# Kernel tuning notes

Hardware: AMD Instinct MI355X
Metric: run time of the kernel (lower is better)

Reference implementation:

```python
import jax, jax.numpy as jnp
import numpy as np

B, S, D, DQKV = 4, 2048, 1024, 1024

def setup_inputs() -> dict:
    key = jax.random.key(0)
    kx, kq, kk, kv = jax.random.split(key, 4)
    scale = 1.0 / np.sqrt(D)
    return {
        "x": jax.random.normal(kx, (B, S, D), dtype=jnp.float32),
        "wq": jax.random.normal(kq, (D, DQKV), dtype=jnp.float32) * scale,
        "wk": jax.random.normal(kk, (D, DQKV), dtype=jnp.float32) * scale,
        "wv": jax.random.normal(kv, (D, DQKV), dtype=jnp.float32) * scale,
    }

def reference(x, wq, wk, wv):
    # QKV projections: [B,S,D] @ [D,Dqkv] -> [B,S,Dqkv]
    q = jnp.einsum('bsd,de->bse', x, wq)
    k = jnp.einsum('bsd,de->bse', x, wk)
    v = jnp.einsum('bsd,de->bse', x, wv)
    # scores: [B,S,S], scaled by sqrt(dim_qkv)
    scores = jnp.einsum('bik,bjk->bij', q, k) / jnp.sqrt(jnp.asarray(DQKV, dtype=x.dtype))
    attn = jax.nn.softmax(scores, axis=-1)
    # output: [B,S,Dqkv]
    return jnp.einsum('bij,bjd->bid', attn, v)
```

## Files before the change

kernel.cpp:

```cpp
#include <hip/hip_runtime.h>
#include <cstdint>
#include <cstddef>

typedef __bf16 bf16;
typedef __bf16 bf16x4 __attribute__((ext_vector_type(4)));
typedef __bf16 bf16x8 __attribute__((ext_vector_type(8)));
typedef float  f32x4  __attribute__((ext_vector_type(4)));
typedef float  f32x16 __attribute__((ext_vector_type(16)));

#define BATCH 4
#define SEQ   2048
#define DIM   1024
#define LDP   2112

__device__ __forceinline__ bf16 to_bf16(float f) {
    unsigned u = __builtin_bit_cast(unsigned, f);
    u += 0x7fffu + ((u >> 16) & 1u);
    unsigned short h = (unsigned short)(u >> 16);
    return __builtin_bit_cast(bf16, h);
}

__device__ __forceinline__ void load16_lds(const bf16* g, bf16* l) {
    __builtin_amdgcn_global_load_lds(
        (__attribute__((address_space(1))) void*)(g),
        (__attribute__((address_space(3))) void*)(l),
        16, 0, 0);
}

__device__ __forceinline__ void stage_tiles(
    const bf16* __restrict__ Abase, const bf16* __restrict__ Bbase,
    int k0, int lda, int ldb, bf16* As, bf16* Bs)
{
    const int tid   = threadIdx.x;
    const int wave  = tid >> 6;
    const int lane  = tid & 63;
    const int srow0 = wave * 8 + (lane >> 3);
    const int scoff = (((lane & 7) ^ ((lane >> 3) & 7)) * 8);
    const int ldsW  = wave * 512;
#pragma unroll
    for (int j = 0; j < 4; ++j) {
        load16_lds(Abase + (size_t)(j * 32 + srow0) * lda + k0 + scoff,
                   As + j * 2048 + ldsW);
        load16_lds(Bbase + (size_t)(j * 32 + srow0) * ldb + k0 + scoff,
                   Bs + j * 2048 + ldsW);
    }
}

__device__ __forceinline__ void gemm_core64_16(
    const bf16* __restrict__ Abase, const bf16* __restrict__ Bbase,
    int K, int lda, int ldb, bf16* As, bf16* Bs, f32x4 acc[4][4])
{
    const int tid  = threadIdx.x;
    const int lane = tid & 63;
    const int wave = tid >> 6;
    const int wm   = (wave >> 1) * 64;
    const int wn   = (wave & 1) * 64;
    const int r16  = lane & 15;
    const int g    = lane >> 4;

    for (int k0 = 0; k0 < K; k0 += 64) {
        __syncthreads();
        stage_tiles(Abase, Bbase, k0, lda, ldb, As, Bs);
        __syncthreads();
#pragma unroll
        for (int h = 0; h < 2; ++h) {
            bf16x8 af[4], bfr[4];
            const int p = (h * 4 + g) ^ (r16 & 7);
#pragma unroll
            for (int i = 0; i < 4; ++i) {
                af[i]  = *(const bf16x8*)(As + (wm + i * 16 + r16) * 64 + p * 8);
                bfr[i] = *(const bf16x8*)(Bs + (wn + i * 16 + r16) * 64 + p * 8);
            }
#pragma unroll
            for (int mi = 0; mi < 4; ++mi)
#pragma unroll
                for (int ni = 0; ni < 4; ++ni)
                    acc[mi][ni] = __builtin_amdgcn_mfma_f32_16x16x32_bf16(
                        af[mi], bfr[ni], acc[mi][ni], 0, 0, 0);
        }
    }
}

__device__ __forceinline__ void gemm_core64_32(
    const bf16* __restrict__ Abase, const bf16* __restrict__ Bbase,
    int K, int lda, int ldb, bf16* As, bf16* Bs, f32x16 acc[2][2])
{
    const int tid  = threadIdx.x;
    const int lane = tid & 63;
    const int wave = tid >> 6;
    const int wm   = (wave >> 1) * 64;
    const int wn   = (wave & 1) * 64;
    const int r32  = lane & 31;
    const int hi   = lane >> 5;

    for (int k0 = 0; k0 < K; k0 += 64) {
        __syncthreads();
        stage_tiles(Abase, Bbase, k0, lda, ldb, As, Bs);
        __syncthreads();
#pragma unroll
        for (int t = 0; t < 4; ++t) {
            bf16x8 af[2], bfr[2];
            const int p = (2 * t + hi) ^ (r32 & 7);
#pragma unroll
            for (int i = 0; i < 2; ++i) {
                af[i]  = *(const bf16x8*)(As + (wm + i * 32 + r32) * 64 + p * 8);
                bfr[i] = *(const bf16x8*)(Bs + (wn + i * 32 + r32) * 64 + p * 8);
            }
#pragma unroll
            for (int mi = 0; mi < 2; ++mi)
#pragma unroll
                for (int ni = 0; ni < 2; ++ni)
                    acc[mi][ni] = __builtin_amdgcn_mfma_f32_32x32x16_bf16(
                        af[mi], bfr[ni], acc[mi][ni], 0, 0, 0);
        }
    }
}

__device__ __forceinline__ int c32_row(int reg, int hi) {
    return (reg & 3) + 8 * (reg >> 2) + 4 * hi;
}

__global__ __launch_bounds__(256, 4) void proj_gemm(
    const bf16* __restrict__ xb, const bf16* __restrict__ Wt,
    bf16* __restrict__ Q, bf16* __restrict__ Kb, bf16* __restrict__ Vt)
{
    __shared__ bf16 As[8192];
    __shared__ bf16 Bs[8192];
    f32x16 acc[2][2] = {};

    const int r = blockIdx.x;
    const bf16 *Ab, *Bb;
    bf16* Cb;
    int ldc;
    if (r < 1024) {
        const int c = r & 7, j = r >> 3;
        const int bx  = j & 15;
        const int byl = c + 8 * (j >> 4);
        Ab = xb + (size_t)byl * 128 * DIM;
        Bb = Wt + (size_t)bx * 128 * DIM;
        bf16* dst = (bx < 8) ? Q : Kb;
        Cb = dst + (size_t)byl * 128 * DIM + (size_t)(bx & 7) * 128;
        ldc = DIM;
    } else {
        const int u = r - 1024;
        const int c = u & 7, j = u >> 3;
        const int bx = j & 15;
        const int p = c + 8 * (j >> 4);
        const int byl = p & 7;
        const int bz = p >> 3;
        Ab = Wt + (size_t)2 * DIM * DIM + (size_t)byl * 128 * DIM;
        Bb = xb + (size_t)bz * SEQ * DIM + (size_t)bx * 128 * DIM;
        Cb = Vt + (size_t)bz * DIM * LDP + (size_t)byl * 128 * LDP + (size_t)bx * 128;
        ldc = LDP;
    }
    gemm_core64_32(Ab, Bb, DIM, DIM, DIM, As, Bs, acc);

    const int lane = threadIdx.x & 63;
    const int wave = threadIdx.x >> 6;
    const int hi = lane >> 5, r32 = lane & 31;
    const int wm = (wave >> 1) * 64, wn = (wave & 1) * 64;
#pragma unroll
    for (int mi = 0; mi < 2; ++mi)
#pragma unroll
        for (int ni = 0; ni < 2; ++ni)
#pragma unroll
            for (int reg = 0; reg < 16; ++reg) {
                const int row = wm + mi * 32 + c32_row(reg, hi);
                const int col = wn + ni * 32 + r32;
                Cb[(size_t)row * ldc + col] = to_bf16(acc[mi][ni][reg]);
            }
}

__global__ __launch_bounds__(256, 4) void gemm_scores(
    const bf16* __restrict__ Q, const bf16* __restrict__ Kb, bf16* __restrict__ P,
    float* __restrict__ lsum)
{
    __shared__ bf16 As[8192];
    __shared__ bf16 Bs[8192];
    f32x4 acc[4][4] = {};

    const int d = blockIdx.x + 16 * (blockIdx.y + 16 * blockIdx.z);
    const int c = d & 7, j = d >> 3;
    const int bx = j & 15;
    const int p = c + 8 * (j >> 4);
    const int by = p & 15, bz = p >> 4;

    const bf16* Ab = Q  + (size_t)bz * SEQ * DIM + (size_t)by * 128 * DIM;
    const bf16* Bb = Kb + (size_t)bz * SEQ * DIM + (size_t)bx * 128 * DIM;
    bf16* Cb = P + (size_t)bz * SEQ * LDP;
    gemm_core64_16(Ab, Bb, DIM, DIM, DIM, As, Bs, acc);

    const int lane = threadIdx.x & 63;
    const int wave = threadIdx.x >> 6;
    const int wm = (wave >> 1) * 64, wn = (wave & 1) * 64;
    const int rowBase = by * 128 + wm + ((lane >> 4) * 4);
    const int colBase = bx * 128 + wn + (lane & 15);

#pragma unroll
    for (int mi = 0; mi < 4; ++mi)
#pragma unroll
        for (int ni = 0; ni < 4; ++ni)
#pragma unroll
            for (int rr = 0; rr < 4; ++rr) {
                const float e = __expf(acc[mi][ni][rr] * 0.03125f);
                acc[mi][ni][rr] = e;
                Cb[(size_t)(rowBase + mi * 16 + rr) * LDP + colBase + ni * 16] =
                    to_bf16(e);
            }

    float* ls = lsum + (size_t)bz * SEQ;
#pragma unroll
    for (int mi = 0; mi < 4; ++mi)
#pragma unroll
        for (int rr = 0; rr < 4; ++rr) {
            float s = acc[mi][0][rr] + acc[mi][1][rr] + acc[mi][2][rr] + acc[mi][3][rr];
            s += __shfl_xor(s, 1);
            s += __shfl_xor(s, 2);
            s += __shfl_xor(s, 4);
            s += __shfl_xor(s, 8);
            if ((lane & 15) == 0)
                atomicAdd(ls + rowBase + mi * 16 + rr, s);
        }
}

__global__ __launch_bounds__(256, 4) void gemm_pv(
    const bf16* __restrict__ P, const bf16* __restrict__ Vt, float* __restrict__ C,
    const float* __restrict__ lsum)
{
    __shared__ bf16 As[8192];
    __shared__ bf16 Bs[8192];
    f32x16 acc[2][2] = {};

    const int d = blockIdx.x + 8 * (blockIdx.y + 16 * blockIdx.z);
    const int c = d & 7, j = d >> 3;
    const int bx = j & 7;
    const int p = c + 8 * (j >> 3);
    const int by = p & 15, bz = p >> 4;

    const bf16* Ab = P  + (size_t)bz * SEQ * LDP + (size_t)by * 128 * LDP;
    const bf16* Bb = Vt + (size_t)bz * DIM * LDP + (size_t)bx * 128 * LDP;
    float* Cb = C + (size_t)bz * SEQ * DIM;
    gemm_core64_32(Ab, Bb, SEQ, LDP, LDP, As, Bs, acc);

    const int lane = threadIdx.x & 63;
    const int wave = threadIdx.x >> 6;
    const int hi = lane >> 5, r32 = lane & 31;
    const int wm = (wave >> 1) * 64, wn = (wave & 1) * 64;
    const int rowBase = by * 128 + wm;
    const int colBase = bx * 128 + wn + r32;
    const float* ls = lsum + (size_t)bz * SEQ;
#pragma unroll
    for (int mi = 0; mi < 2; ++mi)
#pragma unroll
        for (int reg = 0; reg < 16; ++reg) {
            const int row = rowBase + mi * 32 + c32_row(reg, hi);
            const float inv = __builtin_amdgcn_rcpf(ls[row]);
#pragma unroll
            for (int ni = 0; ni < 2; ++ni)
                Cb[(size_t)row * DIM + colBase + ni * 32] = acc[mi][ni][reg] * inv;
        }
}

__global__ __launch_bounds__(256) void prep(
    const float* __restrict__ x,  const float* __restrict__ wq,
    const float* __restrict__ wk, const float* __restrict__ wv,
    bf16* __restrict__ xb, bf16* __restrict__ Wt, float* __restrict__ lsum)
{
    __shared__ float tile[32][33];
    const int b = blockIdx.x;
    const int tid = threadIdx.x;
    if (b < 8192) {
        const size_t i = ((size_t)b * 256 + tid) * 4;
        const float4 v = *(const float4*)(x + i);
        bf16x4 o = { to_bf16(v.x), to_bf16(v.y), to_bf16(v.z), to_bf16(v.w) };
        *(bf16x4*)(xb + i) = o;
    } else if (b < 8192 + 3072) {
        const int t   = b - 8192;
        const int sel = t >> 10;
        const int n0  = (t & 31) * 32;
        const int k0  = ((t >> 5) & 31) * 32;
        const float* w = (sel == 0) ? wq : (sel == 1) ? wk : wv;
        const int tx = tid & 31, ty = tid >> 5;
#pragma unroll
        for (int j = 0; j < 32; j += 8)
            tile[ty + j][tx] = w[(size_t)(k0 + ty + j) * 1024 + n0 + tx];
        __syncthreads();
        bf16* dst = Wt + (size_t)sel * 1024 * 1024;
#pragma unroll
        for (int j = 0; j < 32; j += 8)
            dst[(size_t)(n0 + ty + j) * 1024 + k0 + tx] = to_bf16(tile[tx][ty + j]);
    } else {
#pragma unroll
        for (int i = 0; i < 32; ++i)
            lsum[i * 256 + tid] = 0.0f;
    }
}

extern "C" void kernel_launch(void* const* d_in, const int* in_sizes, int n_in,
                              void* d_out, int out_size, void* d_ws, size_t ws_size,
                              hipStream_t stream)
{
    const float* x  = (const float*)d_in[0];
    const float* wq = (const float*)d_in[1];
    const float* wk = (const float*)d_in[2];
    const float* wv = (const float*)d_in[3];
    float* out = (float*)d_out;
    char* ws = (char*)d_ws;

    bf16*  xb   = (bf16*)(ws);
    bf16*  Wt   = (bf16*)(ws + (16u << 20));
    bf16*  Q    = (bf16*)(ws + (22u << 20));
    bf16*  Kb   = (bf16*)(ws + (38u << 20));
    bf16*  Vt   = (bf16*)(ws + (54u << 20));
    bf16*  P    = (bf16*)(ws + (72u << 20));
    float* lsum = (float*)(ws + (108u << 20));

    prep<<<dim3(8192 + 3072 + 1), dim3(256), 0, stream>>>(
        x, wq, wk, wv, xb, Wt, lsum);

    proj_gemm<<<dim3(1536), dim3(256), 0, stream>>>(xb, Wt, Q, Kb, Vt);

    gemm_scores<<<dim3(16, 16, 4), dim3(256), 0, stream>>>(Q, Kb, P, lsum);

    gemm_pv<<<dim3(8, 16, 4), dim3(256), 0, stream>>>(P, Vt, out, lsum);
}
```

Measured before the change: 254.4 us.

## Use 256x256 eight-wave pipelined GEMM core for projection and score kernels

Replaces the 128x128 four-wave GEMM tiles in the QKV projection and QK^T score kernels with a 256x256 tile run by 512 threads. The new core double-buffers LDS, issues the next tile's global-to-LDS loads in quarters between MFMA groups, and uses explicit vmcnt waits, barriers and setprio. This is meant to raise data reuse and hide load latency. In exchange it uses far more LDS per block, launches fewer blocks (384 and 256), and relies on hand-placed waitcnt synchronisation that could race if the counts are wrong.

```diff
diff --git a/kernel.cpp b/kernel.cpp
--- a/kernel.cpp
+++ b/kernel.cpp
@@ -25,6 +25,129 @@
         (__attribute__((address_space(1))) void*)(g),
         (__attribute__((address_space(3))) void*)(l),
         16, 0, 0);
+}
+
+#define BARRIER() do { asm volatile("" ::: "memory"); \
+                       __builtin_amdgcn_s_barrier();  \
+                       asm volatile("" ::: "memory"); } while (0)
+#define LGKM0()   do { asm volatile("s_waitcnt lgkmcnt(0)" ::: "memory"); \
+                       __builtin_amdgcn_sched_barrier(0); } while (0)
+#define VM4()     asm volatile("s_waitcnt vmcnt(4)" ::: "memory")
+#define VM0()     asm volatile("s_waitcnt vmcnt(0)" ::: "memory")
+
+
+__device__ __forceinline__ void stage_half(
+    const bf16* __restrict__ srcRow0, int ld, int k0, bf16* dstHalfBase)
+{
+    const int tid  = threadIdx.x;
+    const int wave = tid >> 6;
+    const int lane = tid & 63;
+    const int rg   = lane >> 3;
+    const int scoff = ((lane & 7) ^ rg) * 8;
+#pragma unroll
+    for (int j = 0; j < 2; ++j) {
+        const int r = wave * 16 + j * 8;
+        load16_lds(srcRow0 + (size_t)(r + rg) * ld + k0 + scoff,
+                   dstHalfBase + r * 64);
+    }
+}
+
+template<int MB, int NB>
+__device__ __forceinline__ void mfma_quad(
+    const bf16x8 a[4][2], const bf16x8 b[4][2], f32x4 acc[8][4])
+{
+    __builtin_amdgcn_s_setprio(1);
+#pragma unroll
+    for (int m = 0; m < 4; ++m)
+#pragma unroll
+        for (int n = 0; n < 2; ++n)
+#pragma unroll
+            for (int ks = 0; ks < 2; ++ks)
+                acc[MB + m][NB + n] = __builtin_amdgcn_mfma_f32_16x16x32_bf16(
+                    a[m][ks], b[NB + n][ks], acc[MB + m][NB + n], 0, 0, 0);
+    __builtin_amdgcn_s_setprio(0);
+}
+
+__device__ __forceinline__ void gemm8_core(
+    const bf16* __restrict__ Ablk, const bf16* __restrict__ Bblk,
+    int K, int lda, int ldb, bf16* As, bf16* Bs, f32x4 acc[8][4])
+{
+    const int tid  = threadIdx.x;
+    const int lane = tid & 63;
+    const int wave = tid >> 6;
+    const int wr   = wave >> 2;
+    const int wc   = wave & 3;
+    const int r16  = lane & 15;
+    const int g    = lane >> 4;
+    const int r7   = r16 & 7;
+    const int pk0  = ((g) ^ r7) * 8;
+    const int pk1  = ((4 + g) ^ r7) * 8;
+    const int arow = (wr * 128 + r16) * 64;
+    const int brow = (wc * 64 + r16) * 64;
+    const int NT   = K >> 6;
+
+    stage_half(Bblk, ldb, 0, Bs);
+    stage_half(Ablk, lda, 0, As);
+    stage_half(Bblk + (size_t)128 * ldb, ldb, 0, Bs + 8192);
+    stage_half(Ablk + (size_t)128 * lda, lda, 0, As + 8192);
+    stage_half(Bblk, ldb, 64, Bs + 16384);
+    stage_half(Ablk, lda, 64, As + 16384);
+    VM4();
+    BARRIER();
+
+    bf16x8 a[4][2], b[4][2];
+#pragma unroll 2
+    for (int t = 0; t < NT; ++t) {
+        bf16* Ac = As + (t & 1) * 16384;
+        bf16* Bc = Bs + (t & 1) * 16384;
+        bf16* An = As + ((t + 1) & 1) * 16384;
+        bf16* Bn = Bs + ((t + 1) & 1) * 16384;
+        const int k1 = (t + 1) << 6;
+        const int k2 = (t + 2) << 6;
+
+#pragma unroll
+        for (int m = 0; m < 4; ++m) {
+            a[m][0] = *(const bf16x8*)(Ac + arow + m * 1024 + pk0);
+            a[m][1] = *(const bf16x8*)(Ac + arow + m * 1024 + pk1);
+        }
+#pragma unroll
+        for (int n = 0; n < 2; ++n) {
+            b[n][0] = *(const bf16x8*)(Bc + brow + n * 1024 + pk0);
+            b[n][1] = *(const bf16x8*)(Bc + brow + n * 1024 + pk1);
+        }
+        if (t + 1 < NT) stage_half(Bblk + (size_t)128 * ldb, ldb, k1, Bn + 8192);
+        BARRIER(); LGKM0();
+        mfma_quad<0, 0>(a, b, acc);
+        BARRIER();
+
+#pragma unroll
+        for (int n = 2; n < 4; ++n) {
+            b[n][0] = *(const bf16x8*)(Bc + brow + n * 1024 + pk0);
+            b[n][1] = *(const bf16x8*)(Bc + brow + n * 1024 + pk1);
+        }
+        if (t + 1 < NT) stage_half(Ablk + (size_t)128 * lda, lda, k1, An + 8192);
+        BARRIER(); LGKM0();
+        mfma_quad<0, 2>(a, b, acc);
+        BARRIER();
+
+#pragma unroll
+        for (int m = 0; m < 4; ++m) {
+            a[m][0] = *(const bf16x8*)(Ac + arow + 4096 + m * 1024 + pk0);
+            a[m][1] = *(const bf16x8*)(Ac + arow + 4096 + m * 1024 + pk1);
+        }
+        if (t + 2 < NT) stage_half(Bblk, ldb, k2, Bc);
+        BARRIER(); LGKM0();
+        mfma_quad<4, 2>(a, b, acc);
+        BARRIER();
+
+        if (t + 2 < NT) stage_half(Ablk, lda, k2, Ac);
+        BARRIER(); LGKM0();
+        mfma_quad<4, 0>(a, b, acc);
+        if (t + 1 < NT) {
+            if (t + 2 < NT) { VM4(); } else { VM0(); }
+        }
+        BARRIER();
+    }
 }
 
 __device__ __forceinline__ void stage_tiles(
@@ -43,41 +166,6 @@
                    As + j * 2048 + ldsW);
         load16_lds(Bbase + (size_t)(j * 32 + srow0) * ldb + k0 + scoff,
                    Bs + j * 2048 + ldsW);
-    }
-}
-
-__device__ __forceinline__ void gemm_core64_16(
-    const bf16* __restrict__ Abase, const bf16* __restrict__ Bbase,
-    int K, int lda, int ldb, bf16* As, bf16* Bs, f32x4 acc[4][4])
-{
-    const int tid  = threadIdx.x;
-    const int lane = tid & 63;
-    const int wave = tid >> 6;
-    const int wm   = (wave >> 1) * 64;
-    const int wn   = (wave & 1) * 64;
-    const int r16  = lane & 15;
-    const int g    = lane >> 4;
-
-    for (int k0 = 0; k0 < K; k0 += 64) {
-        __syncthreads();
-        stage_tiles(Abase, Bbase, k0, lda, ldb, As, Bs);
-        __syncthreads();
-#pragma unroll
-        for (int h = 0; h < 2; ++h) {
-            bf16x8 af[4], bfr[4];
-            const int p = (h * 4 + g) ^ (r16 & 7);
-#pragma unroll
-            for (int i = 0; i < 4; ++i) {
-                af[i]  = *(const bf16x8*)(As + (wm + i * 16 + r16) * 64 + p * 8);
-                bfr[i] = *(const bf16x8*)(Bs + (wn + i * 16 + r16) * 64 + p * 8);
-            }
-#pragma unroll
-            for (int mi = 0; mi < 4; ++mi)
-#pragma unroll
-                for (int ni = 0; ni < 4; ++ni)
-                    acc[mi][ni] = __builtin_amdgcn_mfma_f32_16x16x32_bf16(
-                        af[mi], bfr[ni], acc[mi][ni], 0, 0, 0);
-        }
     }
 }
 
@@ -120,106 +208,91 @@
     return (reg & 3) + 8 * (reg >> 2) + 4 * hi;
 }
 
-__global__ __launch_bounds__(256, 4) void proj_gemm(
+__global__ __launch_bounds__(512, 2) void proj_gemm8(
     const bf16* __restrict__ xb, const bf16* __restrict__ Wt,
     bf16* __restrict__ Q, bf16* __restrict__ Kb, bf16* __restrict__ Vt)
 {
-    __shared__ bf16 As[8192];
-    __shared__ bf16 Bs[8192];
-    f32x16 acc[2][2] = {};
+    __shared__ bf16 As[32768];
+    __shared__ bf16 Bs[32768];
+    f32x4 acc[8][4] = {};
 
     const int r = blockIdx.x;
     const bf16 *Ab, *Bb;
     bf16* Cb;
     int ldc;
-    if (r < 1024) {
-        const int c = r & 7, j = r >> 3;
-        const int bx  = j & 15;
-        const int byl = c + 8 * (j >> 4);
-        Ab = xb + (size_t)byl * 128 * DIM;
-        Bb = Wt + (size_t)bx * 128 * DIM;
-        bf16* dst = (bx < 8) ? Q : Kb;
-        Cb = dst + (size_t)byl * 128 * DIM + (size_t)(bx & 7) * 128;
+    if (r < 256) {
+        const int my = r >> 3, j = r & 7;
+        Ab = xb + (size_t)my * 256 * DIM;
+        Bb = Wt + (size_t)((j >> 2) ? DIM * DIM : 0) + (size_t)(j & 3) * 256 * DIM;
+        bf16* dst = (j >> 2) ? Kb : Q;
+        Cb = dst + (size_t)my * 256 * DIM + (size_t)(j & 3) * 256;
         ldc = DIM;
     } else {
-        const int u = r - 1024;
-        const int c = u & 7, j = u >> 3;
-        const int bx = j & 15;
-        const int p = c + 8 * (j >> 4);
-        const int byl = p & 7;
-        const int bz = p >> 3;
-        Ab = Wt + (size_t)2 * DIM * DIM + (size_t)byl * 128 * DIM;
-        Bb = xb + (size_t)bz * SEQ * DIM + (size_t)bx * 128 * DIM;
-        Cb = Vt + (size_t)bz * DIM * LDP + (size_t)byl * 128 * LDP + (size_t)bx * 128;
+        const int u = r - 256;
+        const int bz = u >> 5, w = u & 31;
+        const int vy = w >> 3, vx = w & 7;
+        Ab = Wt + (size_t)2 * DIM * DIM + (size_t)vy * 256 * DIM;
+        Bb = xb + (size_t)bz * SEQ * DIM + (size_t)vx * 256 * DIM;
+        Cb = Vt + (size_t)bz * DIM * LDP + (size_t)vy * 256 * LDP + (size_t)vx * 256;
         ldc = LDP;
     }
-    gemm_core64_32(Ab, Bb, DIM, DIM, DIM, As, Bs, acc);
+    gemm8_core(Ab, Bb, DIM, DIM, DIM, As, Bs, acc);
 
     const int lane = threadIdx.x & 63;
     const int wave = threadIdx.x >> 6;
-    const int hi = lane >> 5, r32 = lane & 31;
-    const int wm = (wave >> 1) * 64, wn = (wave & 1) * 64;
-#pragma unroll
-    for (int mi = 0; mi < 2; ++mi)
-#pragma unroll
-        for (int ni = 0; ni < 2; ++ni)
-#pragma unroll
-            for (int reg = 0; reg < 16; ++reg) {
-                const int row = wm + mi * 32 + c32_row(reg, hi);
-                const int col = wn + ni * 32 + r32;
-                Cb[(size_t)row * ldc + col] = to_bf16(acc[mi][ni][reg]);
-            }
-}
-
-__global__ __launch_bounds__(256, 4) void gemm_scores(
-    const bf16* __restrict__ Q, const bf16* __restrict__ Kb, bf16* __restrict__ P,
-    float* __restrict__ lsum)
-{
-    __shared__ bf16 As[8192];
-    __shared__ bf16 Bs[8192];
-    f32x4 acc[4][4] = {};
-
-    const int d = blockIdx.x + 16 * (blockIdx.y + 16 * blockIdx.z);
-    const int c = d & 7, j = d >> 3;
-    const int bx = j & 15;
-    const int p = c + 8 * (j >> 4);
-    const int by = p & 15, bz = p >> 4;
-
-    const bf16* Ab = Q  + (size_t)bz * SEQ * DIM + (size_t)by * 128 * DIM;
-    const bf16* Bb = Kb + (size_t)bz * SEQ * DIM + (size_t)bx * 128 * DIM;
-    bf16* Cb = P + (size_t)bz * SEQ * LDP;
-    gemm_core64_16(Ab, Bb, DIM, DIM, DIM, As, Bs, acc);
-
+    const int wr = wave >> 2, wc = wave & 3;
+    const int r16 = lane & 15, g = lane >> 4;
+    const int row0 = wr * 128 + g * 4;
+    const int col0 = wc * 64 + r16;
+#pragma unroll
+    for (int m = 0; m < 8; ++m)
+#pragma unroll
+        for (int n = 0; n < 4; ++n)
+#pragma unroll
+            for (int rr = 0; rr < 4; ++rr)
+                Cb[(size_t)(row0 + m * 16 + rr) * ldc + col0 + n * 16] =
+                    to_bf16(acc[m][n][rr]);
+}
+
+__global__ __launch_bounds__(512, 2) void gemm_scores8(
+    const bf16* __restrict__ Qm, const bf16* __restrict__ Kb,
+    bf16* __restrict__ P, float* __restrict__ lsum)
+{
+    __shared__ bf16 As[32768];
+    __shared__ bf16 Bs[32768];
+    f32x4 acc[8][4] = {};
+
+    const int d = blockIdx.x;
+    const int bx = d & 7, by = (d >> 3) & 7, bz = d >> 6;
+    const bf16* Ab = Qm + (size_t)bz * SEQ * DIM + (size_t)by * 256 * DIM;
+    const bf16* Bb = Kb + (size_t)bz * SEQ * DIM + (size_t)bx * 256 * DIM;
+    gemm8_core(Ab, Bb, DIM, DIM, DIM, As, Bs, acc);
+
+    bf16* Cb  = P + (size_t)bz * SEQ * LDP;
+    float* ls = lsum + (size_t)bz * SEQ;
     const int lane = threadIdx.x & 63;
     const int wave = threadIdx.x >> 6;
-    const int wm = (wave >> 1) * 64, wn = (wave & 1) * 64;
-    const int rowBase = by * 128 + wm + ((lane >> 4) * 4);
-    const int colBase = bx * 128 + wn + (lane & 15);
-
-#pragma unroll
-    for (int mi = 0; mi < 4; ++mi)
-#pragma unroll
-        for (int ni = 0; ni < 4; ++ni)
-#pragma unroll
-            for (int rr = 0; rr < 4; ++rr) {
-                const float e = __expf(acc[mi][ni][rr] * 0.03125f);
-                acc[mi][ni][rr] = e;
-                Cb[(size_t)(rowBase + mi * 16 + rr) * LDP + colBase + ni * 16] =
-                    to_bf16(e);
+    const int wr = wave >> 2, wc = wave & 3;
+    const int r16 = lane & 15, g = lane >> 4;
+    const int rowB = by * 256 + wr * 128 + g * 4;
+    const int colB = bx * 256 + wc * 64 + r16;
+#pragma unroll
+    for (int m = 0; m < 8; ++m)
+#pragma unroll
+        for (int rr = 0; rr < 4; ++rr) {
+            float s = 0.0f;
+#pragma unroll
+            for (int n = 0; n < 4; ++n) {
+                const float e = __expf(acc[m][n][rr] * 0.03125f);
+                s += e;
+                Cb[(size_t)(rowB + m * 16 + rr) * LDP + colB + n * 16] = to_bf16(e);
             }
-
-    float* ls = lsum + (size_t)bz * SEQ;
-#pragma unroll
-    for (int mi = 0; mi < 4; ++mi)
-#pragma unroll
-        for (int rr = 0; rr < 4; ++rr) {
-            float s = acc[mi][0][rr] + acc[mi][1][rr] + acc[mi][2][rr] + acc[mi][3][rr];
             s += __shfl_xor(s, 1);
             s += __shfl_xor(s, 2);
             s += __shfl_xor(s, 4);
             s += __shfl_xor(s, 8);
-            if ((lane & 15) == 0)
-                atomicAdd(ls + rowBase + mi * 16 + rr, s);
+            if (r16 == 0)
+                atomicAdd(ls + rowB + m * 16 + rr, s);
         }
 }
 
@@ -318,9 +391,9 @@
     prep<<<dim3(8192 + 3072 + 1), dim3(256), 0, stream>>>(
         x, wq, wk, wv, xb, Wt, lsum);
 
-    proj_gemm<<<dim3(1536), dim3(256), 0, stream>>>(xb, Wt, Q, Kb, Vt);
-
-    gemm_scores<<<dim3(16, 16, 4), dim3(256), 0, stream>>>(Q, Kb, P, lsum);
+    proj_gemm8<<<dim3(384), dim3(512), 0, stream>>>(xb, Wt, Q, Kb, Vt);
+
+    gemm_scores8<<<dim3(256), dim3(512), 0, stream>>>(Q, Kb, P, lsum);
 
     gemm_pv<<<dim3(8, 16, 4), dim3(256), 0, stream>>>(P, Vt, out, lsum);
 }
```

After: 247.4 us. -2.8%, faster.
